# Optimization experiments

Measured on AMD Instinct MI355X. Metric: run time of the kernel, lower is better.

The kernel has to match this reference:

```python
import jax, jax.numpy as jnp
import numpy as np

# Mamba-2 config (from MambaBackbone defaults)
D_MODEL = 512
D_STATE = 64
D_CONV = 4
EXPAND = 2
HEADDIM = 64
CHUNK = 256
D_INNER = EXPAND * D_MODEL            # 1024
NHEADS = D_INNER // HEADDIM           # 16
CONV_DIM = D_INNER + 2 * D_STATE      # 1152 (ngroups=1)
D_IN_PROJ = 2 * D_INNER + 2 * D_STATE + NHEADS  # 2192


def setup_inputs() -> dict:
    key = jax.random.key(0)
    ks = jax.random.split(key, 8)
    B, T = 4, 4096
    x = jax.random.normal(ks[0], (B, T, D_MODEL), dtype=jnp.float32)
    W_in = jax.random.normal(ks[1], (D_IN_PROJ, D_MODEL), dtype=jnp.float32) * 0.02
    conv_w = jax.random.normal(ks[2], (CONV_DIM, D_CONV), dtype=jnp.float32) * 0.2
    conv_b = jnp.zeros((CONV_DIM,), jnp.float32)
    # dt_bias initialized so softplus(dt_bias) ~ Uniform-log[1e-3, 1e-1] (mamba2 init)
    dt0 = jnp.exp(jax.random.uniform(ks[3], (NHEADS,)) * (np.log(0.1) - np.log(0.001)) + np.log(0.001))
    dt_bias = dt0 + jnp.log(-jnp.expm1(-dt0))
    A_log = jnp.log(jnp.arange(1, NHEADS + 1, dtype=jnp.float32))  # A = -exp(A_log) in [-16,-1]
    D = jnp.ones((NHEADS,), jnp.float32)
    norm_w = jnp.ones((D_INNER,), jnp.float32)
    W_out = jax.random.normal(ks[4], (D_MODEL, D_INNER), dtype=jnp.float32) * 0.02
    return dict(x=x, W_in=W_in, conv_w=conv_w, conv_b=conv_b, dt_bias=dt_bias,
                A_log=A_log, D=D, norm_w=norm_w, W_out=W_out)


def segsum(a):
    """a: (..., l) -> (..., l, l) with [i,j] = sum_{j<k<=i} a[..,k]; -inf above diag."""
    l = a.shape[-1]
    cs = jnp.cumsum(a, axis=-1)
    ss = cs[..., :, None] - cs[..., None, :]
    mask = jnp.tril(jnp.ones((l, l), dtype=bool))
    return jnp.where(mask, ss, -jnp.inf)


def reference(x, W_in, conv_w, conv_b, dt_bias, A_log, D, norm_w, W_out):
    Bb, T, _ = x.shape
    # input projection -> [z | xBC | dt]
    zxbcdt = x @ W_in.T                                    # (B,T,2192)
    z = zxbcdt[..., :D_INNER]
    xBC = zxbcdt[..., D_INNER:D_INNER + CONV_DIM]
    dt = zxbcdt[..., -NHEADS:]
    # causal depthwise conv1d (kernel D_CONV) + SiLU
    xp = jnp.pad(xBC, ((0, 0), (D_CONV - 1, 0), (0, 0)))
    conv = sum(xp[:, k:k + T, :] * conv_w[:, k] for k in range(D_CONV)) + conv_b
    xBC = jax.nn.silu(conv)
    xs = xBC[..., :D_INNER].reshape(Bb, T, NHEADS, HEADDIM)  # (B,T,H,P)
    Bm = xBC[..., D_INNER:D_INNER + D_STATE]                 # (B,T,N)  ngroups=1
    Cm = xBC[..., D_INNER + D_STATE:]                        # (B,T,N)
    dt = jax.nn.softplus(dt + dt_bias)                       # (B,T,H)
    A = -jnp.exp(A_log)                                      # (H,)
    # ---- chunked SSD (Mamba-2) ----
    nc = T // CHUNK
    Ad = (dt * A).reshape(Bb, nc, CHUNK, NHEADS).transpose(0, 3, 1, 2)   # (b,h,c,l) log-decay
    x_dt = (xs * dt[..., None]).reshape(Bb, nc, CHUNK, NHEADS, HEADDIM)  # (b,c,l,h,p)
    Bc = Bm.reshape(Bb, nc, CHUNK, D_STATE)                              # (b,c,l,n)
    Cc = Cm.reshape(Bb, nc, CHUNK, D_STATE)
    A_cs = jnp.cumsum(Ad, axis=-1)                                       # (b,h,c,l)
    L = jnp.exp(segsum(Ad))                                              # (b,h,c,l,l)
    # intra-chunk (diagonal blocks)
    Y_diag = jnp.einsum('bcln,bcsn,bhcls,bcshp->bclhp', Cc, Bc, L, x_dt)
    # per-chunk end states
    decay_states = jnp.exp(A_cs[..., -1:] - A_cs)                        # (b,h,c,l)
    states = jnp.einsum('bcln,bhcl,bclhp->cbhpn', Bc, decay_states, x_dt)
    chunk_decay = jnp.exp(A_cs[..., -1]).transpose(2, 0, 1)              # (c,b,h)
    def step(h, inp):
        dec, st = inp
        return dec[..., None, None] * h + st, h                          # emit state BEFORE chunk
    h0 = jnp.zeros_like(states[0])
    _, prev = jax.lax.scan(step, h0, (chunk_decay, states))              # (c,b,h,p,n)
    # inter-chunk contribution
    Y_off = jnp.einsum('bcln,cbhpn,bhcl->bclhp', Cc, prev, jnp.exp(A_cs))
    y = (Y_diag + Y_off).reshape(Bb, T, NHEADS, HEADDIM) + D[None, None, :, None] * xs
    y = y.reshape(Bb, T, D_INNER)
    # gated RMSNorm: rmsnorm(y * silu(z)) * w   (norm_before_gate=False)
    yz = y * jax.nn.silu(z)
    out = yz * jax.lax.rsqrt(jnp.mean(yz * yz, axis=-1, keepdims=True) + 1e-5) * norm_w
    return out @ W_out.T
```

## Files before the change

### kernel.cpp

```cpp
#include <hip/hip_runtime.h>
#include <hip/hip_bf16.h>
#include <cstdint>

typedef unsigned int  uint;
typedef unsigned short ushort;
using bf16 = __hip_bfloat16;

#define B_     4
#define T_     4096
#define DM     512
#define DI     1024
#define DSTATE 64
#define HD     64
#define NH     16
#define NC     16
#define CHK    256
#define CONVD  1152
#define DPROJ  2192

using f32x4 = __attribute__((ext_vector_type(4))) float;
using s16x8 = __attribute__((ext_vector_type(8))) short;

#define MFMA16(a, b, c) __builtin_amdgcn_mfma_f32_16x16x32_bf16((a), (b), (c), 0, 0, 0)

__device__ inline void unpack8(const uint4 v, float* f) {
  const uint w[4] = {v.x, v.y, v.z, v.w};
#pragma unroll
  for (int i = 0; i < 4; ++i) {
    f[2*i]   = __uint_as_float(w[i] << 16);
    f[2*i+1] = __uint_as_float(w[i] & 0xffff0000u);
  }
}
__device__ inline void unpack4(const uint2 v, float* f) {
  f[0] = __uint_as_float(v.x << 16); f[1] = __uint_as_float(v.x & 0xffff0000u);
  f[2] = __uint_as_float(v.y << 16); f[3] = __uint_as_float(v.y & 0xffff0000u);
}
__device__ inline ushort bfbits(float a) {
  bf16 h = __float2bfloat16(a);
  return *reinterpret_cast<ushort*>(&h);
}
__device__ inline uint pack2(float a, float b) {
  return (uint)bfbits(a) | ((uint)bfbits(b) << 16);
}
__device__ inline uint4 pack8(const float* f) {
  uint4 v;
  v.x = pack2(f[0], f[1]); v.y = pack2(f[2], f[3]);
  v.z = pack2(f[4], f[5]); v.w = pack2(f[6], f[7]);
  return v;
}

__device__ __forceinline__ void gl_lds16(const void* g, void* l) {
  __builtin_amdgcn_global_load_lds(
      (const __attribute__((address_space(1))) unsigned int*)g,
      (__attribute__((address_space(3))) unsigned int*)l, 16, 0, 0);
}

__global__ __launch_bounds__(256)
void cast_bf16(const float* __restrict__ in, short* __restrict__ out, int n8) {
  const int i = blockIdx.x * 256 + threadIdx.x;
  if (i >= n8) return;
  float f[8];
  float4 a = *reinterpret_cast<const float4*>(&in[(size_t)i * 8]);
  float4 b = *reinterpret_cast<const float4*>(&in[(size_t)i * 8 + 4]);
  f[0]=a.x; f[1]=a.y; f[2]=a.z; f[3]=a.w; f[4]=b.x; f[5]=b.y; f[6]=b.z; f[7]=b.w;
  *reinterpret_cast<uint4*>(&out[(size_t)i * 8]) = pack8(f);
}

template<int EPI>
__global__ __launch_bounds__(256)
void gemm_mfma(const short* __restrict__ A, const short* __restrict__ Bw,
               int K, int N, int nbx, float* __restrict__ Cout,
               short* __restrict__ z, short* __restrict__ xbc,
               float* __restrict__ dtr) {
  __shared__ __align__(16) char smem[(EPI == 1) ? 34816 : 32768];
  short* As = reinterpret_cast<short*>(smem);
  short* Bs = As + 128 * 64;
  const int tid  = threadIdx.x;
  const int lane = tid & 63, w = tid >> 6;
  const int hi = lane >> 4, lo = lane & 15;
  const int lx = lo & 7;
  const int wr = w >> 1, wc = w & 1;

  const int cpx = gridDim.x >> 3;
  const int swz = (blockIdx.x & 7) * cpx + (blockIdx.x >> 3);
  const int bm = (swz / nbx) * 128, bn = (swz % nbx) * 128;

  f32x4 acc[4][4] = {};

  const int srow = lane >> 3;
  const int scol = ((lane & 7) ^ srow) * 8;

  for (int k0 = 0; k0 < K; k0 += 64) {
#pragma unroll
    for (int i = 0; i < 4; ++i) {
      const int seg = w * 4 + i;
      const int row = seg * 8 + srow;
      gl_lds16(&A[(size_t)(bm + row) * K + k0 + scol], &As[seg * 512]);
      const int brow = (bn + row < N) ? (bn + row) : (N - 1);
      gl_lds16(&Bw[(size_t)brow * K + k0 + scol], &Bs[seg * 512]);
    }
    __syncthreads();
#pragma unroll
    for (int kb = 0; kb < 2; ++kb) {
      s16x8 af[4], bf[4];
#pragma unroll
      for (int t = 0; t < 4; ++t) {
        const int gg = ((kb * 4 + hi) ^ lx) * 8;
        af[t] = *reinterpret_cast<const s16x8*>(&As[(wr*64 + t*16 + lo) * 64 + gg]);
        bf[t] = *reinterpret_cast<const s16x8*>(&Bs[(wc*64 + t*16 + lo) * 64 + gg]);
      }
#pragma unroll
      for (int lt = 0; lt < 4; ++lt)
#pragma unroll
        for (int nt = 0; nt < 4; ++nt)
          acc[lt][nt] = MFMA16(af[lt], bf[nt], acc[lt][nt]);
    }
    __syncthreads();
  }

  if (EPI == 0) {
#pragma unroll
    for (int lt = 0; lt < 4; ++lt)
#pragma unroll
      for (int nt = 0; nt < 4; ++nt) {
        const int cg = bn + wc * 64 + nt * 16 + lo;
#pragma unroll
        for (int r = 0; r < 4; ++r) {
          const int rg = bm + wr * 64 + lt * 16 + hi * 4 + r;
          Cout[(size_t)rg * DM + cg] = acc[lt][nt][r];
        }
      }
  } else {
    if (bn + 128 > DI + CONVD) {
#pragma unroll
      for (int lt = 0; lt < 4; ++lt)
#pragma unroll
        for (int nt = 0; nt < 4; ++nt) {
          const int cg = bn + wc * 64 + nt * 16 + lo;
          if (cg >= DI + CONVD && cg < DPROJ) {
#pragma unroll
            for (int r = 0; r < 4; ++r) {
              const int rg = bm + wr * 64 + lt * 16 + hi * 4 + r;
              dtr[(size_t)rg * NH + (cg - DI - CONVD)] = acc[lt][nt][r];
            }
          }
        }
    }
    ushort (*tile)[136] = reinterpret_cast<ushort(*)[136]>(smem);
    __syncthreads();
#pragma unroll
    for (int lt = 0; lt < 4; ++lt)
#pragma unroll
      for (int nt = 0; nt < 4; ++nt) {
        const int cl = wc * 64 + nt * 16 + lo;
#pragma unroll
        for (int r = 0; r < 4; ++r)
          tile[wr * 64 + lt * 16 + hi * 4 + r][cl] = bfbits(acc[lt][nt][r]);
      }
    __syncthreads();
#pragma unroll
    for (int it = 0; it < 8; ++it) {
      const int unit = it * 256 + tid;
      const int row = unit >> 4;
      const int c8  = (unit & 15) << 3;
      const int cg  = bn + c8;
      const int rg  = bm + row;
      if (cg >= DI + CONVD) continue;
      uint4 v = *reinterpret_cast<const uint4*>(&tile[row][c8]);
      if (cg < DI)
        *reinterpret_cast<uint4*>(&reinterpret_cast<ushort*>(z)[(size_t)rg * DI + cg]) = v;
      else
        *reinterpret_cast<uint4*>(&reinterpret_cast<ushort*>(xbc)[(size_t)rg * CONVD + (cg - DI)]) = v;
    }
  }
}

__global__ __launch_bounds__(256)
void conv_silu(const short* __restrict__ xbc, const float* __restrict__ cw,
               const float* __restrict__ cb, short* __restrict__ xc) {
  const int idx = blockIdx.x * 256 + threadIdx.x;
  const int cp = idx % 576;
  const int tb = idx / 576;
  const int ch = cp * 2;
  const int b  = tb >> 9;
  const int t0 = (tb & 511) << 3;
  const long base = ((long)b * T_ + t0) * CONVD + ch;

  const float4 wa = *reinterpret_cast<const float4*>(&cw[ch * 4]);
  const float4 wb = *reinterpret_cast<const float4*>(&cw[ch * 4 + 4]);
  const float ba = cb[ch], bb = cb[ch + 1];

  float va[11], vb[11];
#pragma unroll
  for (int i = 0; i < 11; ++i) {
    const int t = t0 - 3 + i;
    if (t >= 0) {
      const uint u = *reinterpret_cast<const uint*>(&xbc[base + (long)(i - 3) * CONVD]);
      va[i] = __uint_as_float(u << 16);
      vb[i] = __uint_as_float(u & 0xffff0000u);
    } else { va[i] = 0.f; vb[i] = 0.f; }
  }
#pragma unroll
  for (int j = 0; j < 8; ++j) {
    float sa = ba + va[j]*wa.x + va[j+1]*wa.y + va[j+2]*wa.z + va[j+3]*wa.w;
    float sb = bb + vb[j]*wb.x + vb[j+1]*wb.y + vb[j+2]*wb.z + vb[j+3]*wb.w;
    sa = sa / (1.f + __expf(-sa));
    sb = sb / (1.f + __expf(-sb));
    *reinterpret_cast<uint*>(&xc[base + (long)j * CONVD]) = pack2(sa, sb);
  }
}

__global__ __launch_bounds__(256)
void dt_softplus(const float* __restrict__ dtr, const float* __restrict__ dt_bias,
                 float* __restrict__ dtp) {
  const int idx = blockIdx.x * 256 + threadIdx.x;
  const int h = idx & 15;
  const float v = dtr[idx] + dt_bias[h];
  dtp[idx] = (v > 20.f) ? v : log1pf(expf(v));
}

__global__ __launch_bounds__(256, 2)
void ssd_chunk_mfma(const short* __restrict__ xc, const float* __restrict__ dtp,
                    const float* __restrict__ A_log, const float* __restrict__ Dvec,
                    float* __restrict__ acs_g, float* __restrict__ states,
                    short* __restrict__ y) {
  const int blk = blockIdx.x;
  const int h = blk & 15, c = (blk >> 4) & 15, b = blk >> 8;
  const int tid = threadIdx.x;
  const int lane = tid & 63, w = tid >> 6;
  const int hi = lane >> 4, lo = lane & 15;

  __shared__ __align__(16) float acs[CHK];
  __shared__ __align__(16) short Bsm[64][72];
  __shared__ __align__(16) short Btm[64][72];
  __shared__ __align__(16) short Xtm[64][72];
  __shared__ __align__(16) short Xdm[64][72];
  __shared__ __align__(16) short Pb[4][64][72];

  const size_t row0 = (size_t)b * T_ + (size_t)c * CHK;

  const float Ah = -expf(A_log[h]);
  acs[tid] = dtp[(row0 + tid) * NH + h] * Ah;
  __syncthreads();
#pragma unroll
  for (int off = 1; off < CHK; off <<= 1) {
    const float v = acs[tid];
    const float u = (tid >= off) ? acs[tid - off] : 0.f;
    __syncthreads();
    acs[tid] = v + u;
    __syncthreads();
  }
  acs_g[(((size_t)b * NH + h) * NC + c) * CHK + tid] = acs[tid];
  const float acs_last = acs[CHK - 1];

  s16x8 creg[4][2];
#pragma unroll
  for (int lt = 0; lt < 4; ++lt)
#pragma unroll
    for (int kb = 0; kb < 2; ++kb)
      creg[lt][kb] = *reinterpret_cast<const s16x8*>(
          &xc[(row0 + w*64 + lt*16 + lo) * CONVD + DI + DSTATE + kb*32 + hi*8]);

  f32x4 yacc[4][4] = {};
  f32x4 stacc[4]   = {};

  const int sr = tid >> 2;
  const int q  = tid & 3;

  for (int ss = 0; ss < 4; ++ss) {
    const int s0 = ss * 64;
    {
      const size_t gr = (row0 + s0 + sr) * (size_t)CONVD;
      const float dval = dtp[(row0 + s0 + sr) * NH + h];
      const float ddec = __expf(acs_last - acs[s0 + sr]);
      uint4 b0 = *reinterpret_cast<const uint4*>(&xc[gr + DI + q*16]);
      uint4 b1 = *reinterpret_cast<const uint4*>(&xc[gr + DI + q*16 + 8]);
      *reinterpret_cast<uint4*>(&Bsm[sr][q*16])     = b0;
      *reinterpret_cast<uint4*>(&Bsm[sr][q*16 + 8]) = b1;
      const short* bb0 = reinterpret_cast<const short*>(&b0);
      const short* bb1 = reinterpret_cast<const short*>(&b1);
#pragma unroll
      for (int j = 0; j < 8; ++j) Btm[q*16 + j][sr]     = bb0[j];
#pragma unroll
      for (int j = 0; j < 8; ++j) Btm[q*16 + 8 + j][sr] = bb1[j];
      uint4 x0 = *reinterpret_cast<const uint4*>(&xc[gr + h*HD + q*16]);
      uint4 x1 = *reinterpret_cast<const uint4*>(&xc[gr + h*HD + q*16 + 8]);
      float xf[16]; unpack8(x0, xf); unpack8(x1, xf + 8);
#pragma unroll
      for (int j = 0; j < 16; ++j) {
        const float xd = xf[j] * dval;
        Xtm[q*16 + j][sr] = (short)bfbits(xd);
        Xdm[q*16 + j][sr] = (short)bfbits(xd * ddec);
      }
    }
    __syncthreads();

    if (ss <= w) {
      f32x4 sacc[4][4] = {};
#pragma unroll
      for (int kb = 0; kb < 2; ++kb) {
        s16x8 bfr[4];
#pragma unroll
        for (int st = 0; st < 4; ++st)
          bfr[st] = *reinterpret_cast<const s16x8*>(&Bsm[st*16 + lo][kb*32 + hi*8]);
#pragma unroll
        for (int lt = 0; lt < 4; ++lt)
#pragma unroll
          for (int st = 0; st < 4; ++st)
            sacc[lt][st] = MFMA16(bfr[st], creg[lt][kb], sacc[lt][st]);
      }
#pragma unroll
      for (int lt = 0; lt < 4; ++lt) {
        const int l = w*64 + lt*16 + lo;
        const float al = acs[l];
#pragma unroll
        for (int st = 0; st < 4; ++st) {
          float p4[4];
#pragma unroll
          for (int r = 0; r < 4; ++r) {
            const int s = s0 + st*16 + hi*4 + r;
            const float wgt = (s <= l) ? __expf(al - acs[s]) : 0.f;
            p4[r] = sacc[lt][st][r] * wgt;
          }
          uint2 pk; pk.x = pack2(p4[0], p4[1]); pk.y = pack2(p4[2], p4[3]);
          *reinterpret_cast<uint2*>(&Pb[w][lt*16 + lo][st*16 + hi*4]) = pk;
        }
      }
#pragma unroll
      for (int kb = 0; kb < 2; ++kb) {
        s16x8 xfr[4], pfr[4];
#pragma unroll
        for (int pt = 0; pt < 4; ++pt)
          xfr[pt] = *reinterpret_cast<const s16x8*>(&Xtm[pt*16 + lo][kb*32 + hi*8]);
#pragma unroll
        for (int lt = 0; lt < 4; ++lt)
          pfr[lt] = *reinterpret_cast<const s16x8*>(&Pb[w][lt*16 + lo][kb*32 + hi*8]);
#pragma unroll
        for (int pt = 0; pt < 4; ++pt)
#pragma unroll
          for (int lt = 0; lt < 4; ++lt)
            yacc[pt][lt] = MFMA16(xfr[pt], pfr[lt], yacc[pt][lt]);
      }
    }
#pragma unroll
    for (int kb = 0; kb < 2; ++kb) {
      s16x8 xdf = *reinterpret_cast<const s16x8*>(&Xdm[w*16 + lo][kb*32 + hi*8]);
#pragma unroll
      for (int nt = 0; nt < 4; ++nt) {
        s16x8 btf = *reinterpret_cast<const s16x8*>(&Btm[nt*16 + lo][kb*32 + hi*8]);
        stacc[nt] = MFMA16(xdf, btf, stacc[nt]);
      }
    }
    __syncthreads();
  }

  const float Dh = Dvec[h];
#pragma unroll
  for (int lt = 0; lt < 4; ++lt) {
    const int l = w*64 + lt*16 + lo;
    ushort* yrow = reinterpret_cast<ushort*>(&y[(row0 + l) * DI + h * HD]);
    const short* xrow = &xc[(row0 + l) * CONVD + h * HD];
#pragma unroll
    for (int pt = 0; pt < 4; ++pt) {
      const int p0 = pt*16 + hi*4;
      uint2 xb2 = *reinterpret_cast<const uint2*>(&xrow[p0]);
      float xf[4]; unpack4(xb2, xf);
      float o[4];
#pragma unroll
      for (int r = 0; r < 4; ++r) o[r] = yacc[pt][lt][r] + Dh * xf[r];
      uint2 pk; pk.x = pack2(o[0], o[1]); pk.y = pack2(o[2], o[3]);
      *reinterpret_cast<uint2*>(&yrow[p0]) = pk;
    }
  }
  {
    const size_t sbase = (((size_t)c * B_ + b) * NH + h) * (HD * DSTATE);
#pragma unroll
    for (int nt = 0; nt < 4; ++nt) {
      const int n = nt*16 + lo;
#pragma unroll
      for (int r = 0; r < 4; ++r) {
        const int p = w*16 + hi*4 + r;
        states[sbase + (size_t)p * DSTATE + n] = stacc[nt][r];
      }
    }
  }
}

__global__ __launch_bounds__(256)
void chunk_scan(const float* __restrict__ acs_g, const float* __restrict__ st,
                short* __restrict__ pv) {
  const int idx = blockIdx.x * 256 + threadIdx.x;
  const int pn = idx & 4095;
  const int h  = (idx >> 12) & 15;
  const int b  = idx >> 16;
  float hst = 0.f;
#pragma unroll
  for (int c = 0; c < NC; ++c) {
    const size_t o = (((size_t)c * B_ + b) * NH + h) * 4096 + pn;
    reinterpret_cast<ushort*>(pv)[o] = bfbits(hst);
    const float dec = __expf(acs_g[(((size_t)b * NH + h) * NC + c) * CHK + CHK - 1]);
    hst = dec * hst + st[o];
  }
}

__global__ __launch_bounds__(256)
void yoff_mfma(const short* __restrict__ xc, const float* __restrict__ acs_g,
               const short* __restrict__ pv, short* __restrict__ y) {
  const int blk = blockIdx.x;
  const int h = blk & 15, c = (blk >> 4) & 15, b = blk >> 8;
  const int tid = threadIdx.x;
  const int lane = tid & 63, w = tid >> 6;
  const int hi = lane >> 4, lo = lane & 15;
  const size_t row0 = (size_t)b * T_ + (size_t)c * CHK;
  const float* ac = &acs_g[(((size_t)b * NH + h) * NC + c) * CHK];
  const short* pvb = &pv[(((size_t)c * B_ + b) * NH + h) * 4096];

  s16x8 creg[4][2];
#pragma unroll
  for (int lt = 0; lt < 4; ++lt)
#pragma unroll
    for (int kb = 0; kb < 2; ++kb)
      creg[lt][kb] = *reinterpret_cast<const s16x8*>(
          &xc[(row0 + w*64 + lt*16 + lo) * CONVD + DI + DSTATE + kb*32 + hi*8]);

  f32x4 acc[4][4] = {};
#pragma unroll
  for (int kb = 0; kb < 2; ++kb) {
    s16x8 pf[4];
#pragma unroll
    for (int pt = 0; pt < 4; ++pt)
      pf[pt] = *reinterpret_cast<const s16x8*>(&pvb[(pt*16 + lo) * DSTATE + kb*32 + hi*8]);
#pragma unroll
    for (int pt = 0; pt < 4; ++pt)
#pragma unroll
      for (int lt = 0; lt < 4; ++lt)
        acc[pt][lt] = MFMA16(pf[pt], creg[lt][kb], acc[pt][lt]);
  }
#pragma unroll
  for (int lt = 0; lt < 4; ++lt) {
    const int l = w*64 + lt*16 + lo;
    const float el = __expf(ac[l]);
    ushort* yrow = reinterpret_cast<ushort*>(&y[(row0 + l) * DI + h * HD]);
#pragma unroll
    for (int pt = 0; pt < 4; ++pt) {
      const int p0 = pt*16 + hi*4;
      uint2 cur = *reinterpret_cast<const uint2*>(&yrow[p0]);
      float f[4]; unpack4(cur, f);
#pragma unroll
      for (int r = 0; r < 4; ++r) f[r] += el * acc[pt][lt][r];
      uint2 pk; pk.x = pack2(f[0], f[1]); pk.y = pack2(f[2], f[3]);
      *reinterpret_cast<uint2*>(&yrow[p0]) = pk;
    }
  }
}

__global__ __launch_bounds__(256)
void gate_rmsnorm(const short* __restrict__ z, const float* __restrict__ norm_w,
                  short* __restrict__ y) {
  const int row = blockIdx.x;
  const int tid = threadIdx.x;
  const short* zrow = &z[(size_t)row * DI];
  short* yrow = &y[(size_t)row * DI];
  uint2 yb = *reinterpret_cast<const uint2*>(&yrow[tid * 4]);
  uint2 zb = *reinterpret_cast<const uint2*>(&zrow[tid * 4]);
  float yv[4], zv[4];
  unpack4(yb, yv); unpack4(zb, zv);
  float tq[4];
  float ss = 0.f;
#pragma unroll
  for (int j = 0; j < 4; ++j) {
    const float sil = zv[j] / (1.f + __expf(-zv[j]));
    tq[j] = yv[j] * sil;
    ss += tq[j] * tq[j];
  }
#pragma unroll
  for (int off = 32; off >= 1; off >>= 1) ss += __shfl_down(ss, off);
  __shared__ float red[4];
  if ((tid & 63) == 0) red[tid >> 6] = ss;
  __syncthreads();
  const float tot = red[0] + red[1] + red[2] + red[3];
  const float r = rsqrtf(tot * (1.f / (float)DI) + 1e-5f);
  float4 wv = *reinterpret_cast<const float4*>(&norm_w[tid * 4]);
  uint2 ob;
  ob.x = pack2(tq[0] * r * wv.x, tq[1] * r * wv.y);
  ob.y = pack2(tq[2] * r * wv.z, tq[3] * r * wv.w);
  *reinterpret_cast<uint2*>(&yrow[tid * 4]) = ob;
}

extern "C" void kernel_launch(void* const* d_in, const int* in_sizes, int n_in,
                              void* d_out, int out_size, void* d_ws, size_t ws_size,
                              hipStream_t stream) {
  const float* x       = (const float*)d_in[0];
  const float* W_in    = (const float*)d_in[1];
  const float* conv_w  = (const float*)d_in[2];
  const float* conv_b  = (const float*)d_in[3];
  const float* dt_bias = (const float*)d_in[4];
  const float* A_log   = (const float*)d_in[5];
  const float* Dv      = (const float*)d_in[6];
  const float* norm_w  = (const float*)d_in[7];
  const float* W_out   = (const float*)d_in[8];
  float* out = (float*)d_out;

  char* w0 = (char*)d_ws;
  short* z    = (short*)(w0);
  short* xbc  = (short*)(w0 + 33554432ULL);
  short* xc   = (short*)(w0 + 71303168ULL);
  short* wob  = (short*)(w0 + 109051904ULL);
  float* dtr  = (float*)(w0 + 110100480ULL);
  float* dtp  = (float*)(w0 + 111149056ULL);
  float* acs  = (float*)(w0 + 112197632ULL);
  float* st   = (float*)(w0 + 113246208ULL);
  short* pv   = (short*)(w0 + 130023424ULL);
  short* xb   = xc;
  short* wb   = (short*)st;
  short* y    = xbc;

  const int M = B_ * T_;

  cast_bf16<<<(M * DM / 8 + 255) / 256, 256, 0, stream>>>(x, xb, M * DM / 8);
  cast_bf16<<<(DPROJ * DM / 8 + 255) / 256, 256, 0, stream>>>(W_in, wb, DPROJ * DM / 8);
  cast_bf16<<<(DM * DI / 8 + 255) / 256, 256, 0, stream>>>(W_out, wob, DM * DI / 8);

  const int nbx_in = (DPROJ + 127) / 128;
  gemm_mfma<1><<<nbx_in * (M / 128), 256, 0, stream>>>(
      xb, wb, DM, DPROJ, nbx_in, nullptr, z, xbc, dtr);
  conv_silu<<<(M / 8) * 576 / 256, 256, 0, stream>>>(xbc, conv_w, conv_b, xc);
  dt_softplus<<<(M * NH) / 256, 256, 0, stream>>>(dtr, dt_bias, dtp);
  ssd_chunk_mfma<<<B_ * NC * NH, 256, 0, stream>>>(xc, dtp, A_log, Dv, acs, st, y);
  chunk_scan<<<(B_ * NH * HD * DSTATE) / 256, 256, 0, stream>>>(acs, st, pv);
  yoff_mfma<<<B_ * NC * NH, 256, 0, stream>>>(xc, acs, pv, y);
  gate_rmsnorm<<<M, 256, 0, stream>>>(z, norm_w, y);
  gemm_mfma<0><<<(DM / 128) * (M / 128), 256, 0, stream>>>(
      y, wob, DI, DM, DM / 128, out, nullptr, nullptr, nullptr);
}
```

Baseline: 225.5 us.

## Cut LDS and registers in SSD chunk kernel, use wave-shuffle scan

Replaces the barrier-heavy LDS prefix scan with per-wave shuffle scans plus a cross-wave prefix. It shrinks shared memory by dropping the Bsm tile, storing transposed tiles as packed bf16 pairs, and shrinking Pb to one 16-row tile per wave. The S=C·Bᵀ product is now built one l-tile at a time with B fragments read directly from global memory, which lowers register pressure so occupancy can rise to 4 blocks per CU. Block index mapping is changed to put heads outermost so neighbouring blocks share locality, at the cost of more redundant global loads of B.

```diff
diff --git a/kernel.cpp b/kernel.cpp
--- a/kernel.cpp
+++ b/kernel.cpp
@@ -219,38 +219,42 @@
   dtp[idx] = (v > 20.f) ? v : log1pf(expf(v));
 }
 
-__global__ __launch_bounds__(256, 2)
+__global__ __launch_bounds__(256, 4)
 void ssd_chunk_mfma(const short* __restrict__ xc, const float* __restrict__ dtp,
                     const float* __restrict__ A_log, const float* __restrict__ Dvec,
                     float* __restrict__ acs_g, float* __restrict__ states,
                     short* __restrict__ y) {
-  const int blk = blockIdx.x;
-  const int h = blk & 15, c = (blk >> 4) & 15, b = blk >> 8;
+  const int bid = blockIdx.x;
+  const int h = bid >> 6, b = (bid >> 4) & 3, c = bid & 15;
   const int tid = threadIdx.x;
   const int lane = tid & 63, w = tid >> 6;
   const int hi = lane >> 4, lo = lane & 15;
 
   __shared__ __align__(16) float acs[CHK];
-  __shared__ __align__(16) short Bsm[64][72];
-  __shared__ __align__(16) short Btm[64][72];
-  __shared__ __align__(16) short Xtm[64][72];
-  __shared__ __align__(16) short Xdm[64][72];
-  __shared__ __align__(16) short Pb[4][64][72];
+  __shared__ float wsum[4];
+  __shared__ __align__(16) uint Btm2[64 * 36];
+  __shared__ __align__(16) uint Xtm2[64 * 36];
+  __shared__ __align__(16) uint Xdm2[64 * 36];
+  __shared__ __align__(16) short Pb[4][16][72];
 
   const size_t row0 = (size_t)b * T_ + (size_t)c * CHK;
 
   const float Ah = -expf(A_log[h]);
-  acs[tid] = dtp[(row0 + tid) * NH + h] * Ah;
+  float v = dtp[(row0 + tid) * NH + h] * Ah;
+#pragma unroll
+  for (int off = 1; off < 64; off <<= 1) {
+    const float u = __shfl_up(v, off);
+    if (lane >= off) v += u;
+  }
+  if (lane == 63) wsum[w] = v;
   __syncthreads();
-#pragma unroll
-  for (int off = 1; off < CHK; off <<= 1) {
-    const float v = acs[tid];
-    const float u = (tid >= off) ? acs[tid - off] : 0.f;
-    __syncthreads();
-    acs[tid] = v + u;
-    __syncthreads();
-  }
-  acs_g[(((size_t)b * NH + h) * NC + c) * CHK + tid] = acs[tid];
+  float pre = 0.f;
+#pragma unroll
+  for (int ww = 0; ww < 4; ++ww) if (ww < w) pre += wsum[ww];
+  v += pre;
+  acs[tid] = v;
+  acs_g[(((size_t)b * NH + h) * NC + c) * CHK + tid] = v;
+  __syncthreads();
   const float acs_last = acs[CHK - 1];
 
   s16x8 creg[4][2];
@@ -264,91 +268,83 @@
   f32x4 yacc[4][4] = {};
   f32x4 stacc[4]   = {};
 
-  const int sr = tid >> 2;
-  const int q  = tid & 3;
+  const int sp2 = tid & 31;
+  const int g   = tid >> 5;
 
   for (int ss = 0; ss < 4; ++ss) {
     const int s0 = ss * 64;
     {
-      const size_t gr = (row0 + s0 + sr) * (size_t)CONVD;
-      const float dval = dtp[(row0 + s0 + sr) * NH + h];
-      const float ddec = __expf(acs_last - acs[s0 + sr]);
-      uint4 b0 = *reinterpret_cast<const uint4*>(&xc[gr + DI + q*16]);
-      uint4 b1 = *reinterpret_cast<const uint4*>(&xc[gr + DI + q*16 + 8]);
-      *reinterpret_cast<uint4*>(&Bsm[sr][q*16])     = b0;
-      *reinterpret_cast<uint4*>(&Bsm[sr][q*16 + 8]) = b1;
-      const short* bb0 = reinterpret_cast<const short*>(&b0);
-      const short* bb1 = reinterpret_cast<const short*>(&b1);
-#pragma unroll
-      for (int j = 0; j < 8; ++j) Btm[q*16 + j][sr]     = bb0[j];
-#pragma unroll
-      for (int j = 0; j < 8; ++j) Btm[q*16 + 8 + j][sr] = bb1[j];
-      uint4 x0 = *reinterpret_cast<const uint4*>(&xc[gr + h*HD + q*16]);
-      uint4 x1 = *reinterpret_cast<const uint4*>(&xc[gr + h*HD + q*16 + 8]);
-      float xf[16]; unpack8(x0, xf); unpack8(x1, xf + 8);
-#pragma unroll
-      for (int j = 0; j < 16; ++j) {
-        const float xd = xf[j] * dval;
-        Xtm[q*16 + j][sr] = (short)bfbits(xd);
-        Xdm[q*16 + j][sr] = (short)bfbits(xd * ddec);
+      const int se = s0 + 2 * sp2;
+      const size_t re = (row0 + se) * (size_t)CONVD;
+      const size_t ro = re + CONVD;
+      uint4 bqe = *reinterpret_cast<const uint4*>(&xc[re + DI + g*8]);
+      uint4 bqo = *reinterpret_cast<const uint4*>(&xc[ro + DI + g*8]);
+      uint4 xqe = *reinterpret_cast<const uint4*>(&xc[re + h*HD + g*8]);
+      uint4 xqo = *reinterpret_cast<const uint4*>(&xc[ro + h*HD + g*8]);
+      const float de_ = dtp[(row0 + se) * NH + h];
+      const float do_ = dtp[(row0 + se + 1) * NH + h];
+      const float ee = __expf(acs_last - acs[se]);
+      const float eo = __expf(acs_last - acs[se + 1]);
+      const ushort* beu = reinterpret_cast<const ushort*>(&bqe);
+      const ushort* bou = reinterpret_cast<const ushort*>(&bqo);
+      float fe[8], fo[8];
+      unpack8(xqe, fe); unpack8(xqo, fo);
+#pragma unroll
+      for (int j = 0; j < 8; ++j) {
+        const int cidx = (g * 8 + j) * 36 + sp2;
+        Btm2[cidx] = (uint)beu[j] | ((uint)bou[j] << 16);
+        const float te = fe[j] * de_, to = fo[j] * do_;
+        Xtm2[cidx] = pack2(te, to);
+        Xdm2[cidx] = pack2(te * ee, to * eo);
       }
     }
     __syncthreads();
 
+#pragma unroll
+    for (int kb = 0; kb < 2; ++kb) {
+      s16x8 xdf = *reinterpret_cast<const s16x8*>(&Xdm2[(w*16 + lo)*36 + kb*16 + hi*4]);
+#pragma unroll
+      for (int nt = 0; nt < 4; ++nt) {
+        s16x8 btf = *reinterpret_cast<const s16x8*>(&Btm2[(nt*16 + lo)*36 + kb*16 + hi*4]);
+        stacc[nt] = MFMA16(xdf, btf, stacc[nt]);
+      }
+    }
+
     if (ss <= w) {
-      f32x4 sacc[4][4] = {};
-#pragma unroll
-      for (int kb = 0; kb < 2; ++kb) {
-        s16x8 bfr[4];
-#pragma unroll
-        for (int st = 0; st < 4; ++st)
-          bfr[st] = *reinterpret_cast<const s16x8*>(&Bsm[st*16 + lo][kb*32 + hi*8]);
-#pragma unroll
-        for (int lt = 0; lt < 4; ++lt)
-#pragma unroll
-          for (int st = 0; st < 4; ++st)
-            sacc[lt][st] = MFMA16(bfr[st], creg[lt][kb], sacc[lt][st]);
-      }
 #pragma unroll
       for (int lt = 0; lt < 4; ++lt) {
-        const int l = w*64 + lt*16 + lo;
-        const float al = acs[l];
+        f32x4 sacc[4] = {};
+#pragma unroll
+        for (int st = 0; st < 4; ++st) {
+          const short* bsrc = &xc[(row0 + s0 + st*16 + lo) * (size_t)CONVD + DI];
+          s16x8 b0 = *reinterpret_cast<const s16x8*>(&bsrc[hi * 8]);
+          s16x8 b1 = *reinterpret_cast<const s16x8*>(&bsrc[32 + hi * 8]);
+          sacc[st] = MFMA16(b0, creg[lt][0], sacc[st]);
+          sacc[st] = MFMA16(b1, creg[lt][1], sacc[st]);
+        }
+        const int lg = w*64 + lt*16 + lo;
+        const float al = acs[lg];
 #pragma unroll
         for (int st = 0; st < 4; ++st) {
           float p4[4];
 #pragma unroll
           for (int r = 0; r < 4; ++r) {
             const int s = s0 + st*16 + hi*4 + r;
-            const float wgt = (s <= l) ? __expf(al - acs[s]) : 0.f;
-            p4[r] = sacc[lt][st][r] * wgt;
+            const float wgt = (s <= lg) ? __expf(al - acs[s]) : 0.f;
+            p4[r] = sacc[st][r] * wgt;
           }
           uint2 pk; pk.x = pack2(p4[0], p4[1]); pk.y = pack2(p4[2], p4[3]);
-          *reinterpret_cast<uint2*>(&Pb[w][lt*16 + lo][st*16 + hi*4]) = pk;
+          *reinterpret_cast<uint2*>(&Pb[w][lo][st*16 + hi*4]) = pk;
         }
-      }
-#pragma unroll
-      for (int kb = 0; kb < 2; ++kb) {
-        s16x8 xfr[4], pfr[4];
-#pragma unroll
-        for (int pt = 0; pt < 4; ++pt)
-          xfr[pt] = *reinterpret_cast<const s16x8*>(&Xtm[pt*16 + lo][kb*32 + hi*8]);
-#pragma unroll
-        for (int lt = 0; lt < 4; ++lt)
-          pfr[lt] = *reinterpret_cast<const s16x8*>(&Pb[w][lt*16 + lo][kb*32 + hi*8]);
-#pragma unroll
-        for (int pt = 0; pt < 4; ++pt)
-#pragma unroll
-          for (int lt = 0; lt < 4; ++lt)
-            yacc[pt][lt] = MFMA16(xfr[pt], pfr[lt], yacc[pt][lt]);
-      }
-    }
-#pragma unroll
-    for (int kb = 0; kb < 2; ++kb) {
-      s16x8 xdf = *reinterpret_cast<const s16x8*>(&Xdm[w*16 + lo][kb*32 + hi*8]);
-#pragma unroll
-      for (int nt = 0; nt < 4; ++nt) {
-        s16x8 btf = *reinterpret_cast<const s16x8*>(&Btm[nt*16 + lo][kb*32 + hi*8]);
-        stacc[nt] = MFMA16(xdf, btf, stacc[nt]);
+#pragma unroll
+        for (int kb = 0; kb < 2; ++kb) {
+          s16x8 pfr = *reinterpret_cast<const s16x8*>(&Pb[w][lo][kb*32 + hi*8]);
+#pragma unroll
+          for (int pt = 0; pt < 4; ++pt) {
+            s16x8 xfr = *reinterpret_cast<const s16x8*>(&Xtm2[(pt*16 + lo)*36 + kb*16 + hi*4]);
+            yacc[pt][lt] = MFMA16(xfr, pfr, yacc[pt][lt]);
+          }
+        }
       }
     }
     __syncthreads();
@@ -406,8 +402,8 @@
 __global__ __launch_bounds__(256)
 void yoff_mfma(const short* __restrict__ xc, const float* __restrict__ acs_g,
                const short* __restrict__ pv, short* __restrict__ y) {
-  const int blk = blockIdx.x;
-  const int h = blk & 15, c = (blk >> 4) & 15, b = blk >> 8;
+  const int bid = blockIdx.x;
+  const int h = bid >> 6, b = (bid >> 4) & 3, c = bid & 15;
   const int tid = threadIdx.x;
   const int lane = tid & 63, w = tid >> 6;
   const int hi = lane >> 4, lo = lane & 15;
```

New measurement: 361.9 us. +60.5%, slower.
